# Kernel optimization log

Measured on AMD Instinct MI355X. Metric: run time of the kernel, lower is better.

Reference implementation:

```python
import jax, jax.numpy as jnp
import numpy as np

HIDDEN = 2048
HEADS = 16
HEAD_DIM = HIDDEN // HEADS  # 128


def setup_inputs() -> dict:
    key = jax.random.key(0)
    ks = jax.random.split(key, 9)
    B, S = 2, 2048
    x = jax.random.normal(ks[0], (B, S, HIDDEN), dtype=jnp.float32)
    scale = 1.0 / np.sqrt(HIDDEN)
    Wq = jax.random.normal(ks[1], (HIDDEN, HIDDEN), dtype=jnp.float32) * scale
    Wk = jax.random.normal(ks[2], (HIDDEN, HIDDEN), dtype=jnp.float32) * scale
    Wv = jax.random.normal(ks[3], (HIDDEN, HIDDEN), dtype=jnp.float32) * scale
    Wo = jax.random.normal(ks[4], (HIDDEN, HIDDEN), dtype=jnp.float32) * scale
    bq = jnp.zeros((HIDDEN,), dtype=jnp.float32)
    bk = jnp.zeros((HIDDEN,), dtype=jnp.float32)
    bv = jnp.zeros((HIDDEN,), dtype=jnp.float32)
    bo = jnp.zeros((HIDDEN,), dtype=jnp.float32)
    return {"x": x, "Wq": Wq, "bq": bq, "Wk": Wk, "bk": bk,
            "Wv": Wv, "bv": bv, "Wo": Wo, "bo": bo}


def reference(x, Wq, bq, Wk, bk, Wv, bv, Wo, bo):
    B, S, H = x.shape
    nh, hd = HEADS, HEAD_DIM
    # projections: Linear stores W as [out, in], applies x @ W.T + b
    q = (x @ Wq.T + bq).reshape(B, S, nh, hd).transpose(0, 2, 1, 3)  # [B,nh,S,hd]
    k = (x @ Wk.T + bk).reshape(B, S, nh, hd).transpose(0, 2, 1, 3)
    v = (x @ Wv.T + bv).reshape(B, S, nh, hd).transpose(0, 2, 1, 3)
    scores = jnp.einsum("bhqd,bhkd->bhqk", q, k) / np.sqrt(hd)  # [B,nh,S,S]
    causal = jnp.tril(jnp.ones((S, S), dtype=bool))
    scores = jnp.where(causal[None, None], scores, -jnp.inf)
    probs = jax.nn.softmax(scores, axis=-1)
    attn = jnp.einsum("bhqk,bhkd->bhqd", probs, v)  # [B,nh,S,hd]
    y = attn.transpose(0, 2, 1, 3).reshape(B, S, H)
    return y @ Wo.T + bo
```

## Files before the change

### kernel.cpp

```cpp
#include <hip/hip_runtime.h>

#define HIDDEN 2048
#define NH 16
#define HD 128
#define BATCH 2
#define SEQ 2048

typedef __attribute__((ext_vector_type(8))) short short8;
typedef __attribute__((ext_vector_type(4))) float floatx4;

__device__ inline unsigned short f2bf(float f) {
  union { float f; unsigned int u; } x; x.f = f;
  unsigned int r = x.u + 0x7fffu + ((x.u >> 16) & 1u);
  return (unsigned short)(r >> 16);
}
__device__ inline unsigned int pkbf(float a, float b) {
  return (unsigned int)f2bf(a) | ((unsigned int)f2bf(b) << 16);
}

__device__ inline void async_cp16(const void* g, void* l) {
  __builtin_amdgcn_global_load_lds(
      (const __attribute__((address_space(1))) unsigned int*)g,
      (__attribute__((address_space(3))) unsigned int*)l, 16, 0, 0);
}

__global__ __launch_bounds__(256) void cvt_kernel(const float* __restrict__ in,
                                                  unsigned short* __restrict__ out,
                                                  int n) {
  int i = (blockIdx.x * 256 + threadIdx.x) * 4;
  if (i + 3 < n) {
    float4 v = *reinterpret_cast<const float4*>(in + i);
    ushort4 o;
    o.x = f2bf(v.x); o.y = f2bf(v.y); o.z = f2bf(v.z); o.w = f2bf(v.w);
    *reinterpret_cast<ushort4*>(out + i) = o;
  }
}

struct QkvPtrs {
  const unsigned short* W[3];
  const float* b[3];
  unsigned short* oq[3];
  float oscale[3];
};

template<int MODE>
__global__ __launch_bounds__(512, 2) void gemm_nt(const unsigned short* __restrict__ A,
                                                  QkvPtrs P,
                                                  float* __restrict__ outF) {
  __shared__ __align__(16) unsigned short As[2][16384];
  __shared__ __align__(16) unsigned short Bs[2][8192];
  const int t = threadIdx.x;
  const int lane = t & 63;
  const int w = t >> 6;
  const int wr = w >> 1, wc = w & 1;
  const int g = lane >> 4;
  const int l15 = lane & 15;

  const int nwg = gridDim.x;
  int bid = blockIdx.x;
  int Wi = (bid & 7) * (nwg >> 3) + (bid >> 3);
  const int bx = Wi & 15;
  const int byy = Wi >> 4;
  const int wsel = (MODE == 0) ? (byy >> 4) : 0;
  const int row0 = bx * 256;
  const int col0 = (MODE == 0) ? ((byy & 15) * 128) : (byy * 128);

  const unsigned short* Bw = P.W[wsel];
  const float* bias = P.b[wsel];

  floatx4 acc[4][4] = {};

#pragma unroll
  for (int i = 0; i < 4; ++i) {
    int c = t + i * 512;
    async_cp16(A + (size_t)(row0 + (c & 255)) * 2048 + (c >> 8) * 8, &As[0][c * 8]);
  }
#pragma unroll
  for (int i = 0; i < 2; ++i) {
    int c = t + i * 512;
    async_cp16(Bw + (size_t)(col0 + (c & 127)) * 2048 + (c >> 7) * 8, &Bs[0][c * 8]);
  }
  __syncthreads();

  int buf = 0;
  for (int kt = 0; kt < 32; ++kt) {
    if (kt < 31) {
      const int kb = (kt + 1) * 64;
#pragma unroll
      for (int i = 0; i < 4; ++i) {
        int c = t + i * 512;
        async_cp16(A + (size_t)(row0 + (c & 255)) * 2048 + kb + (c >> 8) * 8,
                   &As[buf ^ 1][c * 8]);
      }
#pragma unroll
      for (int i = 0; i < 2; ++i) {
        int c = t + i * 512;
        async_cp16(Bw + (size_t)(col0 + (c & 127)) * 2048 + kb + (c >> 7) * 8,
                   &Bs[buf ^ 1][c * 8]);
      }
    }
    short8 af[2][4], bf[2][4];
#pragma unroll
    for (int ks = 0; ks < 2; ++ks) {
#pragma unroll
      for (int m = 0; m < 4; ++m)
        af[ks][m] = *(const short8*)
            &As[buf][((ks * 4 + g) * 256 + wr * 64 + m * 16 + l15) * 8];
#pragma unroll
      for (int n = 0; n < 4; ++n)
        bf[ks][n] = *(const short8*)
            &Bs[buf][((ks * 4 + g) * 128 + wc * 64 + n * 16 + l15) * 8];
    }
#pragma unroll
    for (int ks = 0; ks < 2; ++ks)
#pragma unroll
      for (int m = 0; m < 4; ++m)
#pragma unroll
        for (int n = 0; n < 4; ++n)
          acc[m][n] = __builtin_amdgcn_mfma_f32_16x16x32_bf16(af[ks][m], bf[ks][n],
                                                              acc[m][n], 0, 0, 0);
    __syncthreads();
    buf ^= 1;
  }

  const float osc = P.oscale[wsel];
#pragma unroll
  for (int m = 0; m < 4; ++m) {
#pragma unroll
    for (int n = 0; n < 4; ++n) {
      int gcol = col0 + wc * 64 + n * 16 + l15;
      float bv = bias[gcol];
#pragma unroll
      for (int r = 0; r < 4; ++r) {
        int grow = row0 + wr * 64 + m * 16 + g * 4 + r;
        float v = acc[m][n][r] + bv;
        if (MODE == 1) {
          outF[(size_t)grow * 2048 + gcol] = v;
        } else {
          int bb = grow >> 11;
          int ss = grow & 2047;
          int hh = gcol >> 7;
          int dd = gcol & 127;
          P.oq[wsel][(((size_t)bb * NH + hh) * SEQ + ss) * HD + dd] = f2bf(v * osc);
        }
      }
    }
  }
}

__global__ __launch_bounds__(256) void attn_kernel(const unsigned short* __restrict__ Q,
                                                   const unsigned short* __restrict__ Kg,
                                                   const unsigned short* __restrict__ Vg,
                                                   unsigned short* __restrict__ O) {
  __shared__ __align__(16) unsigned short Ks[2][16 * 64 * 8];
  __shared__ __align__(16) unsigned short VT[2][8 * 128 * 8];

  const int t = threadIdx.x;
  const int lane = t & 63;
  const int w = t >> 6;
  const int g = lane >> 4;
  const int l15 = lane & 15;

  int gid = blockIdx.x;
  int Wi = (gid < 256) ? gid : 767 - gid;
  const int bx = Wi & 15;
  const int bh = Wi >> 4;
  const int q0 = bx * 128;
  const int bb = bh >> 4;
  const int hh = bh & 15;

  const unsigned short* Qb = Q + (size_t)bh * SEQ * HD;
  const unsigned short* Kb = Kg + (size_t)bh * SEQ * HD;
  const unsigned short* Vb = Vg + (size_t)bh * SEQ * HD;

  const int qw = q0 + w * 32;

  short8 bq[2][4];
#pragma unroll
  for (int qh = 0; qh < 2; ++qh)
#pragma unroll
    for (int kb = 0; kb < 4; ++kb)
      bq[qh][kb] = *(const short8*)(Qb + (size_t)(qw + qh * 16 + l15) * HD + kb * 32 + g * 8);

  floatx4 acc[2][8] = {};
  float mrun[2] = {-1e30f, -1e30f};
  float lrun[2] = {0.f, 0.f};

  short8 vreg[4];
  const int vkv = (t >> 4) * 2;
  const int vd0 = (t & 15) * 8;

  const int ntiles = (q0 >> 6) + 2;

  {
#pragma unroll
    for (int cc = 0; cc < 4; ++cc) {
      int c = t + cc * 256;
      int k8 = c >> 6, s = c & 63;
      int kvs = ((s >> 5) << 5) + (((s >> 2) & 3) << 3) + (((s >> 4) & 1) << 2) + (s & 3);
      async_cp16(Kb + (size_t)kvs * HD + k8 * 8, &Ks[0][c * 8]);
    }
#pragma unroll
    for (int cc = 0; cc < 2; ++cc) {
      vreg[cc * 2]     = *(const short8*)(Vb + (size_t)(vkv + cc * 32) * HD + vd0);
      vreg[cc * 2 + 1] = *(const short8*)(Vb + (size_t)(vkv + cc * 32 + 1) * HD + vd0);
    }
#pragma unroll
    for (int cc = 0; cc < 2; ++cc) {
      int kv = vkv + cc * 32;
      int row = kv >> 3;
#pragma unroll
      for (int j = 0; j < 8; ++j) {
        int d = vd0 + j;
        int dp = d ^ (((d >> 3) ^ row) & 7);
        unsigned int u = (unsigned short)vreg[cc * 2][j] |
                         ((unsigned int)(unsigned short)vreg[cc * 2 + 1][j] << 16);
        *(unsigned int*)&VT[0][(row * 128 + dp) * 8 + (kv & 7)] = u;
      }
    }
    __syncthreads();
  }

  for (int tk = 0; tk < ntiles; ++tk) {
    const int buf = tk & 1;
    const int k0 = tk * 64;
    const bool pf = (tk + 1 < ntiles);

    if (pf) {
      const int kn = k0 + 64;
#pragma unroll
      for (int cc = 0; cc < 4; ++cc) {
        int c = t + cc * 256;
        int k8 = c >> 6, s = c & 63;
        int kvs = ((s >> 5) << 5) + (((s >> 2) & 3) << 3) + (((s >> 4) & 1) << 2) + (s & 3);
        async_cp16(Kb + (size_t)(kn + kvs) * HD + k8 * 8, &Ks[buf ^ 1][c * 8]);
      }
#pragma unroll
      for (int cc = 0; cc < 2; ++cc) {
        vreg[cc * 2]     = *(const short8*)(Vb + (size_t)(kn + vkv + cc * 32) * HD + vd0);
        vreg[cc * 2 + 1] = *(const short8*)(Vb + (size_t)(kn + vkv + cc * 32 + 1) * HD + vd0);
      }
    }

    floatx4 sv[4][2];
#pragma unroll
    for (int kvh = 0; kvh < 4; ++kvh) {
      sv[kvh][0] = (floatx4){0.f, 0.f, 0.f, 0.f};
      sv[kvh][1] = (floatx4){0.f, 0.f, 0.f, 0.f};
#pragma unroll
      for (int kb = 0; kb < 4; ++kb) {
        short8 ak = *(const short8*)&Ks[buf][((kb * 4 + g) * 64 + kvh * 16 + l15) * 8];
        sv[kvh][0] = __builtin_amdgcn_mfma_f32_16x16x32_bf16(ak, bq[0][kb], sv[kvh][0], 0, 0, 0);
        sv[kvh][1] = __builtin_amdgcn_mfma_f32_16x16x32_bf16(ak, bq[1][kb], sv[kvh][1], 0, 0, 0);
      }
    }

    if (k0 + 63 > qw) {
#pragma unroll
      for (int kvh = 0; kvh < 4; ++kvh)
#pragma unroll
        for (int qh = 0; qh < 2; ++qh)
#pragma unroll
          for (int r = 0; r < 4; ++r) {
            int kvg = k0 + ((kvh >> 1) << 5) + g * 8 + ((kvh & 1) << 2) + r;
            int qg = qw + qh * 16 + l15;
            if (kvg > qg) sv[kvh][qh][r] = -1e30f;
          }
    }

#pragma unroll
    for (int qh = 0; qh < 2; ++qh) {
      float mt = sv[0][qh][0];
#pragma unroll
      for (int kvh = 0; kvh < 4; ++kvh)
#pragma unroll
        for (int r = 0; r < 4; ++r)
          mt = fmaxf(mt, sv[kvh][qh][r]);
      mt = fmaxf(mt, __shfl_xor(mt, 16, 64));
      mt = fmaxf(mt, __shfl_xor(mt, 32, 64));
      if (__any(mt > mrun[qh] + 8.0f)) {
        float mnew = fmaxf(mrun[qh], mt);
        float f = __expf(mrun[qh] - mnew);
        mrun[qh] = mnew;
        lrun[qh] *= f;
        float fr[4];
#pragma unroll
        for (int r = 0; r < 4; ++r)
          fr[r] = __shfl(f, (lane & 48) + 4 * g + r, 64);
#pragma unroll
        for (int db = 0; db < 8; ++db)
#pragma unroll
          for (int r = 0; r < 4; ++r)
            acc[qh][db][r] *= fr[r];
      }
      float m = mrun[qh];
      float ssum = 0.f;
#pragma unroll
      for (int kvh = 0; kvh < 4; ++kvh)
#pragma unroll
        for (int r = 0; r < 4; ++r) {
          float p = __expf(sv[kvh][qh][r] - m);
          sv[kvh][qh][r] = p;
          ssum += p;
        }
      ssum += __shfl_xor(ssum, 16, 64);
      ssum += __shfl_xor(ssum, 32, 64);
      lrun[qh] += ssum;
    }

#pragma unroll
    for (int kh = 0; kh < 2; ++kh) {
      union { short8 s8; unsigned int u[4]; } p0, p1;
      p0.u[0] = pkbf(sv[2 * kh][0][0], sv[2 * kh][0][1]);
      p0.u[1] = pkbf(sv[2 * kh][0][2], sv[2 * kh][0][3]);
      p0.u[2] = pkbf(sv[2 * kh + 1][0][0], sv[2 * kh + 1][0][1]);
      p0.u[3] = pkbf(sv[2 * kh + 1][0][2], sv[2 * kh + 1][0][3]);
      p1.u[0] = pkbf(sv[2 * kh][1][0], sv[2 * kh][1][1]);
      p1.u[1] = pkbf(sv[2 * kh][1][2], sv[2 * kh][1][3]);
      p1.u[2] = pkbf(sv[2 * kh + 1][1][0], sv[2 * kh + 1][1][1]);
      p1.u[3] = pkbf(sv[2 * kh + 1][1][2], sv[2 * kh + 1][1][3]);
      int row = kh * 4 + g;
#pragma unroll
      for (int db = 0; db < 8; ++db) {
        int d = db * 16 + l15;
        int dp = d ^ (((d >> 3) ^ row) & 7);
        short8 bv = *(const short8*)&VT[buf][(row * 128 + dp) * 8];
        acc[0][db] = __builtin_amdgcn_mfma_f32_16x16x32_bf16(p0.s8, bv, acc[0][db], 0, 0, 0);
        acc[1][db] = __builtin_amdgcn_mfma_f32_16x16x32_bf16(p1.s8, bv, acc[1][db], 0, 0, 0);
      }
    }

    if (pf) {
#pragma unroll
      for (int cc = 0; cc < 2; ++cc) {
        int kv = vkv + cc * 32;
        int row = kv >> 3;
#pragma unroll
        for (int j = 0; j < 8; ++j) {
          int d = vd0 + j;
          int dp = d ^ (((d >> 3) ^ row) & 7);
          unsigned int u = (unsigned short)vreg[cc * 2][j] |
                           ((unsigned int)(unsigned short)vreg[cc * 2 + 1][j] << 16);
          *(unsigned int*)&VT[buf ^ 1][(row * 128 + dp) * 8 + (kv & 7)] = u;
        }
      }
      __syncthreads();
    }
  }

#pragma unroll
  for (int qh = 0; qh < 2; ++qh) {
    float inv = 1.0f / lrun[qh];
    float ir[4];
#pragma unroll
    for (int r = 0; r < 4; ++r)
      ir[r] = __shfl(inv, (lane & 48) + 4 * g + r, 64);
#pragma unroll
    for (int r = 0; r < 4; ++r) {
      int qg = qw + qh * 16 + 4 * g + r;
      size_t base = ((size_t)bb * SEQ + qg) * HIDDEN + hh * HD;
#pragma unroll
      for (int db = 0; db < 8; ++db)
        O[base + db * 16 + l15] = f2bf(acc[qh][db][r] * ir[r]);
    }
  }
}

extern "C" void kernel_launch(void* const* d_in, const int* in_sizes, int n_in,
                              void* d_out, int out_size, void* d_ws, size_t ws_size,
                              hipStream_t stream) {
  (void)in_sizes; (void)n_in; (void)out_size;
  const float* x  = (const float*)d_in[0];
  const float* Wq = (const float*)d_in[1];
  const float* bq = (const float*)d_in[2];
  const float* Wk = (const float*)d_in[3];
  const float* bk = (const float*)d_in[4];
  const float* Wv = (const float*)d_in[5];
  const float* bv = (const float*)d_in[6];
  const float* Wo = (const float*)d_in[7];
  const float* bo = (const float*)d_in[8];
  float* out = (float*)d_out;

  const float qscale = 0.08838834764831845f;
  char* ws = (char*)d_ws;
  dim3 blk(256);
  dim3 gblk(512);
  const bool fused = ws_size >= 92274688ull;

  if (fused) {
    unsigned short* xbf = (unsigned short*)ws;
    unsigned short* W0  = (unsigned short*)(ws + 16777216);
    unsigned short* W1  = (unsigned short*)(ws + 25165824);
    unsigned short* W2  = (unsigned short*)(ws + 33554432);
    unsigned short* Qbf = (unsigned short*)(ws + 41943040);
    unsigned short* Kbf = (unsigned short*)(ws + 58720256);
    unsigned short* Vbf = (unsigned short*)(ws + 75497472);

    cvt_kernel<<<8192, blk, 0, stream>>>(x, xbf, BATCH * SEQ * HIDDEN);
    cvt_kernel<<<4096, blk, 0, stream>>>(Wq, W0, HIDDEN * HIDDEN);
    cvt_kernel<<<4096, blk, 0, stream>>>(Wk, W1, HIDDEN * HIDDEN);
    cvt_kernel<<<4096, blk, 0, stream>>>(Wv, W2, HIDDEN * HIDDEN);

    QkvPtrs Pq;
    Pq.W[0] = W0;  Pq.W[1] = W1;  Pq.W[2] = W2;
    Pq.b[0] = bq;  Pq.b[1] = bk;  Pq.b[2] = bv;
    Pq.oq[0] = Qbf; Pq.oq[1] = Kbf; Pq.oq[2] = Vbf;
    Pq.oscale[0] = qscale; Pq.oscale[1] = 1.0f; Pq.oscale[2] = 1.0f;
    gemm_nt<0><<<768, gblk, 0, stream>>>(xbf, Pq, nullptr);

    attn_kernel<<<512, blk, 0, stream>>>(Qbf, Kbf, Vbf, xbf);

    cvt_kernel<<<4096, blk, 0, stream>>>(Wo, W0, HIDDEN * HIDDEN);
    QkvPtrs Po;
    Po.W[0] = W0; Po.W[1] = W0; Po.W[2] = W0;
    Po.b[0] = bo; Po.b[1] = bo; Po.b[2] = bo;
    Po.oq[0] = nullptr; Po.oq[1] = nullptr; Po.oq[2] = nullptr;
    Po.oscale[0] = 1.0f; Po.oscale[1] = 1.0f; Po.oscale[2] = 1.0f;
    gemm_nt<1><<<256, gblk, 0, stream>>>(xbf, Po, out);
  } else {
    unsigned short* xbf = (unsigned short*)ws;
    unsigned short* Wbf = (unsigned short*)(ws + 16777216);
    unsigned short* Qbf = (unsigned short*)(ws + 25165824);
    unsigned short* Kbf = (unsigned short*)(ws + 41943040);
    unsigned short* Vbf = (unsigned short*)(ws + 58720256);

    cvt_kernel<<<8192, blk, 0, stream>>>(x, xbf, BATCH * SEQ * HIDDEN);

    const float* biases[3] = {bq, bk, bv};
    const float* wsrc[3] = {Wq, Wk, Wv};
    unsigned short* outs[3] = {Qbf, Kbf, Vbf};
    float oscales[3] = {qscale, 1.0f, 1.0f};
    for (int i = 0; i < 3; ++i) {
      cvt_kernel<<<4096, blk, 0, stream>>>(wsrc[i], Wbf, HIDDEN * HIDDEN);
      QkvPtrs Pp;
      Pp.W[0] = Wbf; Pp.W[1] = Wbf; Pp.W[2] = Wbf;
      Pp.b[0] = biases[i]; Pp.b[1] = biases[i]; Pp.b[2] = biases[i];
      Pp.oq[0] = outs[i]; Pp.oq[1] = outs[i]; Pp.oq[2] = outs[i];
      Pp.oscale[0] = oscales[i]; Pp.oscale[1] = oscales[i]; Pp.oscale[2] = oscales[i];
      gemm_nt<0><<<256, gblk, 0, stream>>>(xbf, Pp, nullptr);
    }

    attn_kernel<<<512, blk, 0, stream>>>(Qbf, Kbf, Vbf, xbf);

    cvt_kernel<<<4096, blk, 0, stream>>>(Wo, Wbf, HIDDEN * HIDDEN);
    QkvPtrs Po;
    Po.W[0] = Wbf; Po.W[1] = Wbf; Po.W[2] = Wbf;
    Po.b[0] = bo; Po.b[1] = bo; Po.b[2] = bo;
    Po.oq[0] = nullptr; Po.oq[1] = nullptr; Po.oq[2] = nullptr;
    Po.oscale[0] = 1.0f; Po.oscale[1] = 1.0f; Po.oscale[2] = 1.0f;
    gemm_nt<1><<<256, gblk, 0, stream>>>(xbf, Po, out);
  }
}
```

Before: 620.7 us.

## Triple-buffer GEMM loads and single-buffer attention with unconditional rescale

The QKV/output GEMM moves from two to three LDS stages, prefetching two k-tiles ahead. It replaces __syncthreads with explicit vmcnt waits plus s_barrier, and raises wave priority around the MFMA block, aiming to hide more global-load latency. The attention kernel drops its double-buffered K/V prefetch and register-staged V for a single LDS buffer loaded synchronously each tile, which may cut register pressure and LDS use but exposes load latency. It also replaces the lazy online-softmax rescale threshold with an unconditional rescale every tile, adding multiplies on the accumulators.

```diff
diff --git a/kernel.cpp b/kernel.cpp
--- a/kernel.cpp
+++ b/kernel.cpp
@@ -47,8 +47,8 @@
 __global__ __launch_bounds__(512, 2) void gemm_nt(const unsigned short* __restrict__ A,
                                                   QkvPtrs P,
                                                   float* __restrict__ outF) {
-  __shared__ __align__(16) unsigned short As[2][16384];
-  __shared__ __align__(16) unsigned short Bs[2][8192];
+  __shared__ __align__(16) unsigned short As[3][16384];
+  __shared__ __align__(16) unsigned short Bs[3][8192];
   const int t = threadIdx.x;
   const int lane = t & 63;
   const int w = t >> 6;
@@ -70,34 +70,35 @@
 
   floatx4 acc[4][4] = {};
 
-#pragma unroll
-  for (int i = 0; i < 4; ++i) {
-    int c = t + i * 512;
-    async_cp16(A + (size_t)(row0 + (c & 255)) * 2048 + (c >> 8) * 8, &As[0][c * 8]);
-  }
-#pragma unroll
-  for (int i = 0; i < 2; ++i) {
-    int c = t + i * 512;
-    async_cp16(Bw + (size_t)(col0 + (c & 127)) * 2048 + (c >> 7) * 8, &Bs[0][c * 8]);
-  }
-  __syncthreads();
-
-  int buf = 0;
+#define STAGE(KT, BUF)                                                              \
+  {                                                                                 \
+    const int kb_ = (KT) * 64;                                                      \
+    _Pragma("unroll")                                                               \
+    for (int i_ = 0; i_ < 4; ++i_) {                                                \
+      int c_ = t + i_ * 512;                                                        \
+      async_cp16(A + (size_t)(row0 + (c_ & 255)) * 2048 + kb_ + (c_ >> 8) * 8,      \
+                 &As[BUF][c_ * 8]);                                                 \
+    }                                                                               \
+    _Pragma("unroll")                                                               \
+    for (int i_ = 0; i_ < 2; ++i_) {                                                \
+      int c_ = t + i_ * 512;                                                        \
+      async_cp16(Bw + (size_t)(col0 + (c_ & 127)) * 2048 + kb_ + (c_ >> 7) * 8,     \
+                 &Bs[BUF][c_ * 8]);                                                 \
+    }                                                                               \
+  }
+
+  STAGE(0, 0);
+  STAGE(1, 1);
+  asm volatile("s_waitcnt vmcnt(6)" ::: "memory");
+  __builtin_amdgcn_s_barrier();
+  __builtin_amdgcn_sched_barrier(0);
+
+  int cb = 0;
   for (int kt = 0; kt < 32; ++kt) {
-    if (kt < 31) {
-      const int kb = (kt + 1) * 64;
-#pragma unroll
-      for (int i = 0; i < 4; ++i) {
-        int c = t + i * 512;
-        async_cp16(A + (size_t)(row0 + (c & 255)) * 2048 + kb + (c >> 8) * 8,
-                   &As[buf ^ 1][c * 8]);
-      }
-#pragma unroll
-      for (int i = 0; i < 2; ++i) {
-        int c = t + i * 512;
-        async_cp16(Bw + (size_t)(col0 + (c & 127)) * 2048 + kb + (c >> 7) * 8,
-                   &Bs[buf ^ 1][c * 8]);
-      }
+    const bool pf = (kt + 2 < 32);
+    if (pf) {
+      const int nb = (cb + 2 >= 3) ? (cb - 1) : (cb + 2);
+      STAGE(kt + 2, nb);
     }
     short8 af[2][4], bf[2][4];
 #pragma unroll
@@ -105,12 +106,13 @@
 #pragma unroll
       for (int m = 0; m < 4; ++m)
         af[ks][m] = *(const short8*)
-            &As[buf][((ks * 4 + g) * 256 + wr * 64 + m * 16 + l15) * 8];
+            &As[cb][((ks * 4 + g) * 256 + wr * 64 + m * 16 + l15) * 8];
 #pragma unroll
       for (int n = 0; n < 4; ++n)
         bf[ks][n] = *(const short8*)
-            &Bs[buf][((ks * 4 + g) * 128 + wc * 64 + n * 16 + l15) * 8];
-    }
+            &Bs[cb][((ks * 4 + g) * 128 + wc * 64 + n * 16 + l15) * 8];
+    }
+    __builtin_amdgcn_s_setprio(1);
 #pragma unroll
     for (int ks = 0; ks < 2; ++ks)
 #pragma unroll
@@ -119,9 +121,16 @@
         for (int n = 0; n < 4; ++n)
           acc[m][n] = __builtin_amdgcn_mfma_f32_16x16x32_bf16(af[ks][m], bf[ks][n],
                                                               acc[m][n], 0, 0, 0);
-    __syncthreads();
-    buf ^= 1;
-  }
+    __builtin_amdgcn_s_setprio(0);
+    if (pf)
+      asm volatile("s_waitcnt vmcnt(6)" ::: "memory");
+    else
+      asm volatile("s_waitcnt vmcnt(0)" ::: "memory");
+    __builtin_amdgcn_s_barrier();
+    __builtin_amdgcn_sched_barrier(0);
+    cb = (cb + 1 >= 3) ? 0 : (cb + 1);
+  }
+#undef STAGE
 
   const float osc = P.oscale[wsel];
 #pragma unroll
@@ -152,8 +161,8 @@
                                                    const unsigned short* __restrict__ Kg,
                                                    const unsigned short* __restrict__ Vg,
                                                    unsigned short* __restrict__ O) {
-  __shared__ __align__(16) unsigned short Ks[2][16 * 64 * 8];
-  __shared__ __align__(16) unsigned short VT[2][8 * 128 * 8];
+  __shared__ __align__(16) unsigned short Ks[16 * 64 * 8];
+  __shared__ __align__(16) unsigned short VT[8 * 128 * 8];
 
   const int t = threadIdx.x;
   const int lane = t & 63;
@@ -186,61 +195,34 @@
   float mrun[2] = {-1e30f, -1e30f};
   float lrun[2] = {0.f, 0.f};
 
-  short8 vreg[4];
-  const int vkv = (t >> 4) * 2;
-  const int vd0 = (t & 15) * 8;
-
   const int ntiles = (q0 >> 6) + 2;
-
-  {
+  for (int tk = 0; tk < ntiles; ++tk) {
+    const int k0 = tk * 64;
+    __syncthreads();
 #pragma unroll
     for (int cc = 0; cc < 4; ++cc) {
       int c = t + cc * 256;
       int k8 = c >> 6, s = c & 63;
       int kvs = ((s >> 5) << 5) + (((s >> 2) & 3) << 3) + (((s >> 4) & 1) << 2) + (s & 3);
-      async_cp16(Kb + (size_t)kvs * HD + k8 * 8, &Ks[0][c * 8]);
+      async_cp16(Kb + (size_t)(k0 + kvs) * HD + k8 * 8, &Ks[c * 8]);
     }
 #pragma unroll
     for (int cc = 0; cc < 2; ++cc) {
-      vreg[cc * 2]     = *(const short8*)(Vb + (size_t)(vkv + cc * 32) * HD + vd0);
-      vreg[cc * 2 + 1] = *(const short8*)(Vb + (size_t)(vkv + cc * 32 + 1) * HD + vd0);
-    }
-#pragma unroll
-    for (int cc = 0; cc < 2; ++cc) {
-      int kv = vkv + cc * 32;
+      int c = t + cc * 256;
+      int kv = (c >> 4) * 2;
+      int d0 = (c & 15) * 8;
       int row = kv >> 3;
+      short8 va = *(const short8*)(Vb + (size_t)(k0 + kv) * HD + d0);
+      short8 vb = *(const short8*)(Vb + (size_t)(k0 + kv + 1) * HD + d0);
 #pragma unroll
       for (int j = 0; j < 8; ++j) {
-        int d = vd0 + j;
+        int d = d0 + j;
         int dp = d ^ (((d >> 3) ^ row) & 7);
-        unsigned int u = (unsigned short)vreg[cc * 2][j] |
-                         ((unsigned int)(unsigned short)vreg[cc * 2 + 1][j] << 16);
-        *(unsigned int*)&VT[0][(row * 128 + dp) * 8 + (kv & 7)] = u;
+        unsigned int u = (unsigned short)va[j] | ((unsigned int)(unsigned short)vb[j] << 16);
+        *(unsigned int*)&VT[(row * 128 + dp) * 8 + (kv & 7)] = u;
       }
     }
     __syncthreads();
-  }
-
-  for (int tk = 0; tk < ntiles; ++tk) {
-    const int buf = tk & 1;
-    const int k0 = tk * 64;
-    const bool pf = (tk + 1 < ntiles);
-
-    if (pf) {
-      const int kn = k0 + 64;
-#pragma unroll
-      for (int cc = 0; cc < 4; ++cc) {
-        int c = t + cc * 256;
-        int k8 = c >> 6, s = c & 63;
-        int kvs = ((s >> 5) << 5) + (((s >> 2) & 3) << 3) + (((s >> 4) & 1) << 2) + (s & 3);
-        async_cp16(Kb + (size_t)(kn + kvs) * HD + k8 * 8, &Ks[buf ^ 1][c * 8]);
-      }
-#pragma unroll
-      for (int cc = 0; cc < 2; ++cc) {
-        vreg[cc * 2]     = *(const short8*)(Vb + (size_t)(kn + vkv + cc * 32) * HD + vd0);
-        vreg[cc * 2 + 1] = *(const short8*)(Vb + (size_t)(kn + vkv + cc * 32 + 1) * HD + vd0);
-      }
-    }
 
     floatx4 sv[4][2];
 #pragma unroll
@@ -249,7 +231,7 @@
       sv[kvh][1] = (floatx4){0.f, 0.f, 0.f, 0.f};
 #pragma unroll
       for (int kb = 0; kb < 4; ++kb) {
-        short8 ak = *(const short8*)&Ks[buf][((kb * 4 + g) * 64 + kvh * 16 + l15) * 8];
+        short8 ak = *(const short8*)&Ks[((kb * 4 + g) * 64 + kvh * 16 + l15) * 8];
         sv[kvh][0] = __builtin_amdgcn_mfma_f32_16x16x32_bf16(ak, bq[0][kb], sv[kvh][0], 0, 0, 0);
         sv[kvh][1] = __builtin_amdgcn_mfma_f32_16x16x32_bf16(ak, bq[1][kb], sv[kvh][1], 0, 0, 0);
       }
@@ -278,34 +260,30 @@
           mt = fmaxf(mt, sv[kvh][qh][r]);
       mt = fmaxf(mt, __shfl_xor(mt, 16, 64));
       mt = fmaxf(mt, __shfl_xor(mt, 32, 64));
-      if (__any(mt > mrun[qh] + 8.0f)) {
-        float mnew = fmaxf(mrun[qh], mt);
-        float f = __expf(mrun[qh] - mnew);
-        mrun[qh] = mnew;
-        lrun[qh] *= f;
-        float fr[4];
-#pragma unroll
-        for (int r = 0; r < 4; ++r)
-          fr[r] = __shfl(f, (lane & 48) + 4 * g + r, 64);
-#pragma unroll
-        for (int db = 0; db < 8; ++db)
-#pragma unroll
-          for (int r = 0; r < 4; ++r)
-            acc[qh][db][r] *= fr[r];
-      }
-      float m = mrun[qh];
+      float mnew = fmaxf(mrun[qh], mt);
+      float f = __expf(mrun[qh] - mnew);
+      mrun[qh] = mnew;
       float ssum = 0.f;
 #pragma unroll
       for (int kvh = 0; kvh < 4; ++kvh)
 #pragma unroll
         for (int r = 0; r < 4; ++r) {
-          float p = __expf(sv[kvh][qh][r] - m);
+          float p = __expf(sv[kvh][qh][r] - mnew);
           sv[kvh][qh][r] = p;
           ssum += p;
         }
       ssum += __shfl_xor(ssum, 16, 64);
       ssum += __shfl_xor(ssum, 32, 64);
-      lrun[qh] += ssum;
+      lrun[qh] = lrun[qh] * f + ssum;
+      float fr[4];
+#pragma unroll
+      for (int r = 0; r < 4; ++r)
+        fr[r] = __shfl(f, (lane & 48) + 4 * g + r, 64);
+#pragma unroll
+      for (int db = 0; db < 8; ++db)
+#pragma unroll
+        for (int r = 0; r < 4; ++r)
+          acc[qh][db][r] *= fr[r];
     }
 
 #pragma unroll
@@ -324,27 +302,10 @@
       for (int db = 0; db < 8; ++db) {
         int d = db * 16 + l15;
         int dp = d ^ (((d >> 3) ^ row) & 7);
-        short8 bv = *(const short8*)&VT[buf][(row * 128 + dp) * 8];
+        short8 bv = *(const short8*)&VT[(row * 128 + dp) * 8];
         acc[0][db] = __builtin_amdgcn_mfma_f32_16x16x32_bf16(p0.s8, bv, acc[0][db], 0, 0, 0);
         acc[1][db] = __builtin_amdgcn_mfma_f32_16x16x32_bf16(p1.s8, bv, acc[1][db], 0, 0, 0);
       }
-    }
-
-    if (pf) {
-#pragma unroll
-      for (int cc = 0; cc < 2; ++cc) {
-        int kv = vkv + cc * 32;
-        int row = kv >> 3;
-#pragma unroll
-        for (int j = 0; j < 8; ++j) {
-          int d = vd0 + j;
-          int dp = d ^ (((d >> 3) ^ row) & 7);
-          unsigned int u = (unsigned short)vreg[cc * 2][j] |
-                           ((unsigned int)(unsigned short)vreg[cc * 2 + 1][j] << 16);
-          *(unsigned int*)&VT[buf ^ 1][(row * 128 + dp) * 8 + (kv & 7)] = u;
-        }
-      }
-      __syncthreads();
     }
   }
 
```

New measurement: 624.7 us. No clear change (+0.7%).
